# Performance work log

Measured on AMD Instinct MI355X. Metric: run time of the kernel, lower is better.

## Reference

```python
import jax, jax.numpy as jnp
import numpy as np

P = 1024          # nodes per graph
B = 64            # graphs in batch
N = P * B         # total nodes
E = N * 32        # total edges (avg degree 32)
D_IN = 16         # per-node feature dim (share_obs_dim)
H = 32            # GCN / MLP hidden dim (hardcoded in GNet)
SHARE = 64        # flat share_state dim


def setup_inputs() -> dict:
    key = jax.random.key(0)
    ks = jax.random.split(key, 20)

    x = jax.random.normal(ks[0], (N, D_IN), jnp.float32)
    src = jax.random.randint(ks[1], (E,), 0, N, dtype=jnp.int32)
    # keep edges inside each 1024-node graph block (PyG batched graphs)
    dst = (src // P) * P + jax.random.randint(ks[2], (E,), 0, P, dtype=jnp.int32)
    edge_index = jnp.stack([src, dst])
    value_batch = (jnp.arange(N, dtype=jnp.int32) // P)
    share_state = jax.random.normal(ks[3], (B, SHARE), jnp.float32)

    def lin(k, o, i):
        return jax.random.normal(k, (o, i), jnp.float32) / np.float32(np.sqrt(i))

    return {
        "x": x, "edge_index": edge_index, "value_batch": value_batch,
        "share_state": share_state,
        # value_gnet: GCNConv(D_IN,32), GCNConv(32,32), Linear(32,32), post-pool Linear(32,32)
        "W1": lin(ks[4], H, D_IN), "b1": jnp.zeros((H,), jnp.float32),
        "W2": lin(ks[5], H, H),    "b2": jnp.zeros((H,), jnp.float32),
        "Wl": lin(ks[6], H, H),    "bl": jnp.zeros((H,), jnp.float32),
        "Wp": lin(ks[7], H, H),    "bp": jnp.zeros((H,), jnp.float32),
        # value_net MLP: SHARE->32->32->32
        "Vw1": lin(ks[8], H, SHARE), "Vb1": jnp.zeros((H,), jnp.float32),
        "Vw2": lin(ks[9], H, H),     "Vb2": jnp.zeros((H,), jnp.float32),
        "Vw3": lin(ks[10], H, H),    "Vb3": jnp.zeros((H,), jnp.float32),
        # value_comnet: 64->32->1
        "Cw1": lin(ks[11], H, 2 * H), "Cb1": jnp.zeros((H,), jnp.float32),
        "Cw2": lin(ks[12], 1, H) * np.float32(0.01), "Cb2": jnp.zeros((1,), jnp.float32),
    }


def gcn_conv(x, src, dst, W, b):
    """PyG GCNConv: D^-1/2 (A+I) D^-1/2 X W^T + b (unit edge weights)."""
    n = x.shape[0]
    loop = jnp.arange(n, dtype=src.dtype)
    s = jnp.concatenate([src, loop])
    d = jnp.concatenate([dst, loop])
    deg = jax.ops.segment_sum(jnp.ones(s.shape[0], x.dtype), d, num_segments=n)
    dis = jnp.where(deg > 0, jax.lax.rsqrt(jnp.maximum(deg, 1e-12)), 0.0)
    norm = dis[s] * dis[d]                      # [E+N]
    h = x @ W.T                                  # [N, H] small GEMM first
    out = jax.ops.segment_sum(h[s] * norm[:, None], d, num_segments=n)
    return out + b


def reference(x, edge_index, value_batch, share_state,
              W1, b1, W2, b2, Wl, bl, Wp, bp,
              Vw1, Vb1, Vw2, Vb2, Vw3, Vb3,
              Cw1, Cb1, Cw2, Cb2):
    src, dst = edge_index[0], edge_index[1]
    nb = share_state.shape[0]

    # value_gnet
    h = jnp.tanh(gcn_conv(x, src, dst, W1, b1))
    h = jnp.tanh(gcn_conv(h, src, dst, W2, b2))
    h = jnp.tanh(h @ Wl.T + bl)
    pooled = jax.ops.segment_sum(h, value_batch, num_segments=nb)  # global_add_pool -> [B, 32]
    h1 = pooled @ Wp.T + bp

    # value_net MLP on flat share_state
    h2 = jnp.tanh(share_state @ Vw1.T + Vb1)
    h2 = jnp.tanh(h2 @ Vw2.T + Vb2)
    h2 = h2 @ Vw3.T + Vb3

    # value_comnet
    z = jnp.tanh(jnp.concatenate([h1, h2], axis=-1) @ Cw1.T + Cb1)
    value = z @ Cw2.T + Cb2                      # [B, 1]
    return value
```

## Files before the change

kernel.cpp:

```cpp
#include <hip/hip_runtime.h>
#include <math.h>

#define NNODES 65536
#define NEDGES 2097152
#define PGRAPH 1024
#define NGRAPH 64
#define CAPE   34560

#define OFF_GFILL 0u
#define OFF_POOL  256u
#define OFF_ROW   8704u
#define OFF_DEG   270848u
#define OFF_DIS   532992u
#define OFF_CSR   795136u
#define OFF_EBUF  5218816u
#define OFF_HBUF  14066176u

__global__ void k_bucket(const int* __restrict__ src, const int* __restrict__ dst,
                         int* __restrict__ gfill, unsigned int* __restrict__ ebuf) {
    __shared__ unsigned int sorted[8192];
    __shared__ int hist[64], lexcl[64], gbase[64], lfill[64];
    int t = threadIdx.x;
    if (t < 64) { hist[t] = 0; lfill[t] = 0; }
    __syncthreads();

    int base = blockIdx.x * 8192;
    unsigned int pk[32];
    int gg[32];
    #pragma unroll
    for (int k = 0; k < 32; k++) {
        int e = base + k * 256 + t;
        int s = src[e], d = dst[e];
        int g = s >> 10;
        pk[k] = (unsigned int)((s & 1023) | ((d & 1023) << 10) | (g << 20));
        gg[k] = g;
        atomicAdd(&hist[g], 1);
    }
    __syncthreads();
    if (t < 64) {
        int h = hist[t];
        int x = h;
        #pragma unroll
        for (int off = 1; off < 64; off <<= 1) {
            int y = __shfl_up(x, off, 64);
            if (t >= off) x += y;
        }
        lexcl[t] = x - h;
        gbase[t] = atomicAdd(&gfill[t], h);
    }
    __syncthreads();
    #pragma unroll
    for (int k = 0; k < 32; k++) {
        int g = gg[k];
        int pos = lexcl[g] + atomicAdd(&lfill[g], 1);
        sorted[pos] = pk[k];
    }
    __syncthreads();
    for (int i = t; i < 8192; i += 256) {
        unsigned int p = sorted[i];
        int g = p >> 20;
        int idx = gbase[g] + (i - lexcl[g]);
        ebuf[(size_t)g * CAPE + idx] = p;
    }
}

__global__ void k_csr(const unsigned int* __restrict__ ebuf, const int* __restrict__ gfill,
                      int* __restrict__ deg, float* __restrict__ dis,
                      int* __restrict__ row_start, unsigned short* __restrict__ csr) {
    __shared__ int ldeg[1024], lrow[1024], lfill[1024];
    __shared__ unsigned short lcsr[CAPE];
    __shared__ int wsum[16];
    int g = blockIdx.x;
    int t = threadIdx.x;
    int cnt = gfill[g];
    const unsigned int* eb = ebuf + (size_t)g * CAPE;

    ldeg[t] = 0;
    __syncthreads();
    for (int i = t; i < cnt; i += 1024) {
        unsigned int v = eb[i];
        atomicAdd(&ldeg[(v >> 10) & 1023], 1);
    }
    __syncthreads();

    int dv = ldeg[t];
    int lane = t & 63, wid = t >> 6;
    int x = dv;
    #pragma unroll
    for (int off = 1; off < 64; off <<= 1) {
        int y = __shfl_up(x, off, 64);
        if (lane >= off) x += y;
    }
    if (lane == 63) wsum[wid] = x;
    __syncthreads();
    if (t < 16) {
        int s = wsum[t];
        #pragma unroll
        for (int off = 1; off < 16; off <<= 1) {
            int y = __shfl_up(s, off, 16);
            if (t >= off) s += y;
        }
        wsum[t] = s;
    }
    __syncthreads();
    int excl = x + ((wid == 0) ? 0 : wsum[wid - 1]) - dv;

    int n = g * PGRAPH + t;
    deg[n] = dv;
    dis[n] = rsqrtf((float)(dv + 1));
    row_start[n] = g * CAPE + excl;
    lrow[t] = excl;
    lfill[t] = 0;
    __syncthreads();

    for (int i = t; i < cnt; i += 1024) {
        unsigned int v = eb[i];
        int s = v & 1023;
        int d = (v >> 10) & 1023;
        int pos = lrow[d] + atomicAdd(&lfill[d], 1);
        lcsr[pos] = (unsigned short)s;
    }
    __syncthreads();
    for (int i = t; i < cnt; i += 1024) csr[(size_t)g * CAPE + i] = lcsr[i];
}

template <int DIN, bool FINAL>
__global__ __launch_bounds__(1024, 1) void k_conv(
        const float* __restrict__ in, const float* __restrict__ W,
        const float* __restrict__ bias, const float* __restrict__ dis,
        const int* __restrict__ row_start, const int* __restrict__ deg,
        const unsigned short* __restrict__ csr,
        const float* __restrict__ Wl, const float* __restrict__ bl,
        float* __restrict__ out) {
    __shared__ float hsL[PGRAPH * 32];
    __shared__ float WlL[32 * 33];
    float4* hsL4 = (float4*)hsL;

    int t = threadIdx.x;
    int g = blockIdx.x >> 2;
    int part = blockIdx.x & 3;

    if (FINAL) { WlL[(t >> 5) * 33 + (t & 31)] = Wl[t]; }

    {
        int n = (g << 10) + t;
        float inr[DIN];
        const float4* in4 = (const float4*)(in + (size_t)n * DIN);
        #pragma unroll
        for (int k = 0; k < DIN / 4; k++) {
            float4 v = in4[k];
            inr[4*k] = v.x; inr[4*k+1] = v.y; inr[4*k+2] = v.z; inr[4*k+3] = v.w;
        }
        float dn = dis[n];
        int sw = t & 7;
        #pragma unroll
        for (int o4 = 0; o4 < 8; o4++) {
            float r[4];
            #pragma unroll
            for (int j = 0; j < 4; j++) {
                int o = o4 * 4 + j;
                float s = 0.f;
                #pragma unroll
                for (int k = 0; k < DIN; k++) s += inr[k] * W[o * DIN + k];
                r[j] = s * dn;
            }
            hsL4[t * 8 + (o4 ^ sw)] = make_float4(r[0], r[1], r[2], r[3]);
        }
    }
    __syncthreads();

    int q = t & 7;
    int grp = t >> 3;
    float4 racc[2];
    #pragma unroll
    for (int pass = 0; pass < 2; pass++) {
        int ln = part * 256 + pass * 128 + grp;
        int nn = (g << 10) + ln;
        float dnd = dis[nn];
        int st = row_start[nn];
        int d  = deg[nn];
        float4 acc = hsL4[ln * 8 + (q ^ (ln & 7))];
        for (int i = 0; i < d; i++) {
            int s = csr[st + i];
            float4 v = hsL4[s * 8 + (q ^ (s & 7))];
            acc.x += v.x; acc.y += v.y; acc.z += v.z; acc.w += v.w;
        }
        float4 bb = ((const float4*)bias)[q];
        float4 r;
        r.x = tanhf(dnd * acc.x + bb.x);
        r.y = tanhf(dnd * acc.y + bb.y);
        r.z = tanhf(dnd * acc.z + bb.z);
        r.w = tanhf(dnd * acc.w + bb.w);
        if (!FINAL) ((float4*)out)[(size_t)nn * 8 + q] = r;
        else        racc[pass] = r;
    }

    if (FINAL) {
        __syncthreads();
        #pragma unroll
        for (int pass = 0; pass < 2; pass++) {
            int lnn = pass * 128 + grp;
            hsL4[lnn * 8 + (q ^ (lnn & 7))] = racc[pass];
        }
        __syncthreads();
        int o = t & 31, seg = t >> 5;
        float ps = 0.f;
        #pragma unroll
        for (int j = 0; j < 8; j++) {
            int nl = seg * 8 + j;
            int swn = nl & 7;
            float s = bl[o];
            #pragma unroll
            for (int k = 0; k < 32; k++) {
                float h2v = hsL[nl * 32 + ((((k >> 2) ^ swn) << 2) | (k & 3))];
                s += h2v * WlL[o * 33 + k];
            }
            ps += tanhf(s);
        }
        float* psum = hsL + 8192;
        psum[t] = ps;
        __syncthreads();
        if (t < 32) {
            float tot = 0.f;
            for (int s = 0; s < 32; s++) tot += psum[s * 32 + t];
            atomicAdd(&out[g * 32 + t], tot);
        }
    }
}

__global__ void k_final(const float* __restrict__ pooled, const float* __restrict__ share,
                        const float* __restrict__ Wp,  const float* __restrict__ bp,
                        const float* __restrict__ Vw1, const float* __restrict__ Vb1,
                        const float* __restrict__ Vw2, const float* __restrict__ Vb2,
                        const float* __restrict__ Vw3, const float* __restrict__ Vb3,
                        const float* __restrict__ Cw1, const float* __restrict__ Cb1,
                        const float* __restrict__ Cw2, const float* __restrict__ Cb2,
                        float* __restrict__ out) {
    int id = blockIdx.x * 256 + threadIdx.x;
    int b = id >> 5;
    int j = id & 31;
    float p = pooled[b * 32 + j];
    float h1v = bp[j];
    #pragma unroll
    for (int k = 0; k < 32; k++) h1v += Wp[j * 32 + k] * __shfl(p, k, 32);
    float s0 = share[b * 64 + j];
    float s1 = share[b * 64 + 32 + j];
    float t1 = Vb1[j];
    #pragma unroll
    for (int k = 0; k < 32; k++) {
        t1 += Vw1[j * 64 + k] * __shfl(s0, k, 32);
        t1 += Vw1[j * 64 + 32 + k] * __shfl(s1, k, 32);
    }
    t1 = tanhf(t1);
    float t2 = Vb2[j];
    #pragma unroll
    for (int k = 0; k < 32; k++) t2 += Vw2[j * 32 + k] * __shfl(t1, k, 32);
    t2 = tanhf(t2);
    float h2v = Vb3[j];
    #pragma unroll
    for (int k = 0; k < 32; k++) h2v += Vw3[j * 32 + k] * __shfl(t2, k, 32);
    float z = Cb1[j];
    #pragma unroll
    for (int k = 0; k < 32; k++) {
        z += Cw1[j * 64 + k] * __shfl(h1v, k, 32);
        z += Cw1[j * 64 + 32 + k] * __shfl(h2v, k, 32);
    }
    z = tanhf(z);
    float v = Cw2[j] * z;
    v += __shfl_down(v, 16, 32); v += __shfl_down(v, 8, 32);
    v += __shfl_down(v, 4, 32);  v += __shfl_down(v, 2, 32);
    v += __shfl_down(v, 1, 32);
    if (j == 0) out[b] = v + Cb2[0];
}

extern "C" void kernel_launch(void* const* d_in, const int* in_sizes, int n_in,
                              void* d_out, int out_size, void* d_ws, size_t ws_size,
                              hipStream_t stream) {
    const float* x     = (const float*)d_in[0];
    const int*   ei    = (const int*)d_in[1];
    const float* share = (const float*)d_in[3];
    const float* W1 = (const float*)d_in[4];  const float* b1 = (const float*)d_in[5];
    const float* W2 = (const float*)d_in[6];  const float* b2 = (const float*)d_in[7];
    const float* Wl = (const float*)d_in[8];  const float* bl = (const float*)d_in[9];
    const float* Wp = (const float*)d_in[10]; const float* bp = (const float*)d_in[11];
    const float* Vw1 = (const float*)d_in[12]; const float* Vb1 = (const float*)d_in[13];
    const float* Vw2 = (const float*)d_in[14]; const float* Vb2 = (const float*)d_in[15];
    const float* Vw3 = (const float*)d_in[16]; const float* Vb3 = (const float*)d_in[17];
    const float* Cw1 = (const float*)d_in[18]; const float* Cb1 = (const float*)d_in[19];
    const float* Cw2 = (const float*)d_in[20]; const float* Cb2 = (const float*)d_in[21];

    char* ws = (char*)d_ws;
    int*            gfill     = (int*)(ws + OFF_GFILL);
    float*          pooled    = (float*)(ws + OFF_POOL);
    int*            row_start = (int*)(ws + OFF_ROW);
    int*            deg       = (int*)(ws + OFF_DEG);
    float*          dis       = (float*)(ws + OFF_DIS);
    unsigned short* csr       = (unsigned short*)(ws + OFF_CSR);
    unsigned int*   ebuf      = (unsigned int*)(ws + OFF_EBUF);
    float*          h1        = (float*)(ws + OFF_HBUF);

    const int* srcp = ei;
    const int* dstp = ei + NEDGES;

    hipMemsetAsync(ws, 0, 8448, stream);

    k_bucket<<<256, 256, 0, stream>>>(srcp, dstp, gfill, ebuf);
    k_csr<<<NGRAPH, 1024, 0, stream>>>(ebuf, gfill, deg, dis, row_start, csr);

    k_conv<16, false><<<256, 1024, 0, stream>>>(x,  W1, b1, dis, row_start, deg, csr,
                                                Wl, bl, h1);
    k_conv<32, true ><<<256, 1024, 0, stream>>>(h1, W2, b2, dis, row_start, deg, csr,
                                                Wl, bl, pooled);
    k_final<<<8, 256, 0, stream>>>(pooled, share, Wp, bp, Vw1, Vb1, Vw2, Vb2,
                                   Vw3, Vb3, Cw1, Cb1, Cw2, Cb2, (float*)d_out);
}
```

Measured before the change: 200.2 us.

## Fuse CSR build into first GCN conv, pad rows, fast tanh, drop pool atomics

Removes the separate CSR-building kernel. Each of the four blocks per graph now builds its own quarter of the CSR in shared memory and runs the first convolution directly from it. Rows are padded to multiples of four with a dummy zero node, so neighbour indices load as ushort4 and gather four rows per iteration. Degree and row start are packed into a single word. tanhf is replaced by an exp/rcp approximation. Pool atomics are replaced by per-block partial sums that k_final adds up. The cost is redundant edge-histogram work: every block scans the whole graph's edge list. It also loses some tanh accuracy.

```diff
diff --git a/kernel.cpp b/kernel.cpp
--- a/kernel.cpp
+++ b/kernel.cpp
@@ -5,16 +5,22 @@
 #define NEDGES 2097152
 #define PGRAPH 1024
 #define NGRAPH 64
-#define CAPE   34560
+#define CAPE_E 34560
+#define CAPQ   9728
+#define CSRG   (4 * CAPQ)
 
 #define OFF_GFILL 0u
-#define OFF_POOL  256u
-#define OFF_ROW   8704u
-#define OFF_DEG   270848u
-#define OFF_DIS   532992u
-#define OFF_CSR   795136u
-#define OFF_EBUF  5218816u
-#define OFF_HBUF  14066176u
+#define OFF_POOL4 256u
+#define OFF_ROWI  33024u
+#define OFF_DIS   295168u
+#define OFF_CSR   557312u
+#define OFF_EBUF  5538048u
+#define OFF_H1    14385408u
+
+__device__ __forceinline__ float ftanh(float x) {
+    float e = __expf(2.f * x);
+    return 1.f - 2.f * __builtin_amdgcn_rcpf(e + 1.f);
+}
 
 __global__ void k_bucket(const int* __restrict__ src, const int* __restrict__ dst,
                          int* __restrict__ gfill, unsigned int* __restrict__ ebuf) {
@@ -24,17 +30,21 @@
     if (t < 64) { hist[t] = 0; lfill[t] = 0; }
     __syncthreads();
 
-    int base = blockIdx.x * 8192;
+    const int4* src4 = (const int4*)(src + blockIdx.x * 8192);
+    const int4* dst4 = (const int4*)(dst + blockIdx.x * 8192);
     unsigned int pk[32];
-    int gg[32];
-    #pragma unroll
-    for (int k = 0; k < 32; k++) {
-        int e = base + k * 256 + t;
-        int s = src[e], d = dst[e];
-        int g = s >> 10;
-        pk[k] = (unsigned int)((s & 1023) | ((d & 1023) << 10) | (g << 20));
-        gg[k] = g;
-        atomicAdd(&hist[g], 1);
+    #pragma unroll
+    for (int k = 0; k < 8; k++) {
+        int4 s4 = src4[k * 256 + t];
+        int4 d4 = dst4[k * 256 + t];
+        int ss[4] = { s4.x, s4.y, s4.z, s4.w };
+        int dd[4] = { d4.x, d4.y, d4.z, d4.w };
+        #pragma unroll
+        for (int j = 0; j < 4; j++) {
+            int g = ss[j] >> 10;
+            pk[k * 4 + j] = (unsigned int)((ss[j] & 1023) | ((dd[j] & 1023) << 10) | (g << 20));
+            atomicAdd(&hist[g], 1);
+        }
     }
     __syncthreads();
     if (t < 64) {
@@ -51,7 +61,7 @@
     __syncthreads();
     #pragma unroll
     for (int k = 0; k < 32; k++) {
-        int g = gg[k];
+        int g = pk[k] >> 20;
         int pos = lexcl[g] + atomicAdd(&lfill[g], 1);
         sorted[pos] = pk[k];
     }
@@ -59,99 +69,91 @@
     for (int i = t; i < 8192; i += 256) {
         unsigned int p = sorted[i];
         int g = p >> 20;
-        int idx = gbase[g] + (i - lexcl[g]);
-        ebuf[(size_t)g * CAPE + idx] = p;
-    }
-}
-
-__global__ void k_csr(const unsigned int* __restrict__ ebuf, const int* __restrict__ gfill,
-                      int* __restrict__ deg, float* __restrict__ dis,
-                      int* __restrict__ row_start, unsigned short* __restrict__ csr) {
-    __shared__ int ldeg[1024], lrow[1024], lfill[1024];
-    __shared__ unsigned short lcsr[CAPE];
-    __shared__ int wsum[16];
-    int g = blockIdx.x;
+        ebuf[(size_t)g * CAPE_E + gbase[g] + (i - lexcl[g])] = p;
+    }
+}
+
+__global__ __launch_bounds__(1024, 1) void k_build_conv1(
+        const float* __restrict__ x, const float* __restrict__ W,
+        const float* __restrict__ bias,
+        const unsigned int* __restrict__ ebuf, const int* __restrict__ gfill,
+        float* __restrict__ disg, unsigned int* __restrict__ rowinfo,
+        unsigned short* __restrict__ csr, float* __restrict__ h1) {
+    __shared__ float hsL[1025 * 32];
+    __shared__ unsigned short lcsr[CAPQ];
+    __shared__ int uhist[1024];
+    __shared__ int lrow[256], lfill[256];
+    __shared__ int wsum[4];
+    float4* hsL4 = (float4*)hsL;
+
     int t = threadIdx.x;
+    int g = blockIdx.x >> 2, part = blockIdx.x & 3;
     int cnt = gfill[g];
-    const unsigned int* eb = ebuf + (size_t)g * CAPE;
-
-    ldeg[t] = 0;
-    __syncthreads();
+    const unsigned int* eb = ebuf + (size_t)g * CAPE_E;
+
+    uhist[t] = 0;
+    if (t < 32) hsL[1024 * 32 + t] = 0.f;
+    __syncthreads();
+    for (int i = t; i < cnt; i += 1024) atomicAdd(&uhist[(eb[i] >> 10) & 1023], 1);
+    __syncthreads();
+
+    int dv_own = uhist[t];
+    float dis_own = rsqrtf((float)(dv_own + 1));
+
+    int dq = 0, r4 = 0;
+    if (t < 256) { dq = uhist[part * 256 + t]; r4 = (dq + 3) & ~3; }
+    int lane = t & 63, wid = t >> 6;
+    int xx = r4;
+    #pragma unroll
+    for (int off = 1; off < 64; off <<= 1) {
+        int y = __shfl_up(xx, off, 64);
+        if (lane >= off) xx += y;
+    }
+    if (t < 256 && lane == 63) wsum[wid] = xx;
+    __syncthreads();
+    if (t < 256) {
+        int pre = 0;
+        for (int w = 0; w < wid; w++) pre += wsum[w];
+        lrow[t] = pre + xx - r4;
+        lfill[t] = 0;
+    }
+    __syncthreads();
+
     for (int i = t; i < cnt; i += 1024) {
         unsigned int v = eb[i];
-        atomicAdd(&ldeg[(v >> 10) & 1023], 1);
-    }
-    __syncthreads();
-
-    int dv = ldeg[t];
-    int lane = t & 63, wid = t >> 6;
-    int x = dv;
-    #pragma unroll
-    for (int off = 1; off < 64; off <<= 1) {
-        int y = __shfl_up(x, off, 64);
-        if (lane >= off) x += y;
-    }
-    if (lane == 63) wsum[wid] = x;
-    __syncthreads();
-    if (t < 16) {
-        int s = wsum[t];
-        #pragma unroll
-        for (int off = 1; off < 16; off <<= 1) {
-            int y = __shfl_up(s, off, 16);
-            if (t >= off) s += y;
-        }
-        wsum[t] = s;
-    }
-    __syncthreads();
-    int excl = x + ((wid == 0) ? 0 : wsum[wid - 1]) - dv;
-
-    int n = g * PGRAPH + t;
-    deg[n] = dv;
-    dis[n] = rsqrtf((float)(dv + 1));
-    row_start[n] = g * CAPE + excl;
-    lrow[t] = excl;
-    lfill[t] = 0;
-    __syncthreads();
-
-    for (int i = t; i < cnt; i += 1024) {
-        unsigned int v = eb[i];
-        int s = v & 1023;
         int d = (v >> 10) & 1023;
-        int pos = lrow[d] + atomicAdd(&lfill[d], 1);
-        lcsr[pos] = (unsigned short)s;
-    }
-    __syncthreads();
-    for (int i = t; i < cnt; i += 1024) csr[(size_t)g * CAPE + i] = lcsr[i];
-}
-
-template <int DIN, bool FINAL>
-__global__ __launch_bounds__(1024, 1) void k_conv(
-        const float* __restrict__ in, const float* __restrict__ W,
-        const float* __restrict__ bias, const float* __restrict__ dis,
-        const int* __restrict__ row_start, const int* __restrict__ deg,
-        const unsigned short* __restrict__ csr,
-        const float* __restrict__ Wl, const float* __restrict__ bl,
-        float* __restrict__ out) {
-    __shared__ float hsL[PGRAPH * 32];
-    __shared__ float WlL[32 * 33];
-    float4* hsL4 = (float4*)hsL;
-
-    int t = threadIdx.x;
-    int g = blockIdx.x >> 2;
-    int part = blockIdx.x & 3;
-
-    if (FINAL) { WlL[(t >> 5) * 33 + (t & 31)] = Wl[t]; }
+        if ((d >> 8) == part) {
+            int dl = d & 255;
+            int pos = lrow[dl] + atomicAdd(&lfill[dl], 1);
+            lcsr[pos] = (unsigned short)(v & 1023);
+        }
+    }
+    __syncthreads();
+    if (t < 256) {
+        int st = lrow[t];
+        for (int i = dq; i < r4; i++) lcsr[st + i] = 1024;
+        int n = (g << 10) + part * 256 + t;
+        disg[n] = rsqrtf((float)(dq + 1));
+        rowinfo[n] = ((unsigned int)st << 16) | (unsigned int)dq;
+    }
+    __syncthreads();
+
+    int qlen = lrow[255] + ((uhist[part * 256 + 255] + 3) & ~3);
+    {
+        const ushort4* l4 = (const ushort4*)lcsr;
+        ushort4* c4 = (ushort4*)(csr + (size_t)g * CSRG + part * CAPQ);
+        for (int i = t; i < (qlen >> 2); i += 1024) c4[i] = l4[i];
+    }
 
     {
         int n = (g << 10) + t;
-        float inr[DIN];
-        const float4* in4 = (const float4*)(in + (size_t)n * DIN);
-        #pragma unroll
-        for (int k = 0; k < DIN / 4; k++) {
+        float inr[16];
+        const float4* in4 = (const float4*)(x + (size_t)n * 16);
+        #pragma unroll
+        for (int k = 0; k < 4; k++) {
             float4 v = in4[k];
             inr[4*k] = v.x; inr[4*k+1] = v.y; inr[4*k+2] = v.z; inr[4*k+3] = v.w;
         }
-        float dn = dis[n];
         int sw = t & 7;
         #pragma unroll
         for (int o4 = 0; o4 < 8; o4++) {
@@ -161,7 +163,82 @@
                 int o = o4 * 4 + j;
                 float s = 0.f;
                 #pragma unroll
-                for (int k = 0; k < DIN; k++) s += inr[k] * W[o * DIN + k];
+                for (int k = 0; k < 16; k++) s += inr[k] * W[o * 16 + k];
+                r[j] = s * dis_own;
+            }
+            hsL4[t * 8 + (o4 ^ sw)] = make_float4(r[0], r[1], r[2], r[3]);
+        }
+    }
+    __syncthreads();
+
+    int q = t & 7, grp = t >> 3;
+    #pragma unroll
+    for (int pass = 0; pass < 2; pass++) {
+        int lq = pass * 128 + grp;
+        int ln = part * 256 + lq;
+        int d = uhist[ln];
+        float dn = rsqrtf((float)(d + 1));
+        int st = lrow[lq];
+        float4 acc = hsL4[ln * 8 + (q ^ (ln & 7))];
+        const ushort4* c4 = (const ushort4*)(lcsr + st);
+        int d4 = (d + 3) >> 2;
+        for (int i = 0; i < d4; i++) {
+            ushort4 ss = c4[i];
+            float4 v0 = hsL4[ss.x * 8 + (q ^ (ss.x & 7))];
+            float4 v1 = hsL4[ss.y * 8 + (q ^ (ss.y & 7))];
+            float4 v2 = hsL4[ss.z * 8 + (q ^ (ss.z & 7))];
+            float4 v3 = hsL4[ss.w * 8 + (q ^ (ss.w & 7))];
+            acc.x += (v0.x + v1.x) + (v2.x + v3.x);
+            acc.y += (v0.y + v1.y) + (v2.y + v3.y);
+            acc.z += (v0.z + v1.z) + (v2.z + v3.z);
+            acc.w += (v0.w + v1.w) + (v2.w + v3.w);
+        }
+        float4 bb = ((const float4*)bias)[q];
+        float4 r;
+        r.x = ftanh(dn * acc.x + bb.x);
+        r.y = ftanh(dn * acc.y + bb.y);
+        r.z = ftanh(dn * acc.z + bb.z);
+        r.w = ftanh(dn * acc.w + bb.w);
+        ((float4*)h1)[((size_t)(g << 10) + ln) * 8 + q] = r;
+    }
+}
+
+__global__ __launch_bounds__(1024, 1) void k_conv2(
+        const float* __restrict__ h1, const float* __restrict__ W,
+        const float* __restrict__ bias, const float* __restrict__ disg,
+        const unsigned int* __restrict__ rowinfo, const unsigned short* __restrict__ csr,
+        const float* __restrict__ Wl, const float* __restrict__ bl,
+        float* __restrict__ pooled4) {
+    __shared__ float hsL[1025 * 32];
+    __shared__ float WlL[32 * 33];
+    float4* hsL4 = (float4*)hsL;
+
+    int t = threadIdx.x;
+    int g = blockIdx.x >> 2, part = blockIdx.x & 3;
+
+    if (t < 32 * 32) WlL[(t >> 5) * 33 + (t & 31)] = Wl[t];
+    if (t < 32) hsL[1024 * 32 + t] = 0.f;
+
+    {
+        int n = (g << 10) + t;
+        float inr[32];
+        const float4* in4 = (const float4*)(h1 + (size_t)n * 32);
+        #pragma unroll
+        for (int k = 0; k < 8; k++) {
+            float4 v = in4[k];
+            inr[4*k] = v.x; inr[4*k+1] = v.y; inr[4*k+2] = v.z; inr[4*k+3] = v.w;
+        }
+        float dn = disg[n];
+        int sw = t & 7;
+        #pragma unroll
+        for (int o4 = 0; o4 < 8; o4++) {
+            float r[4];
+            #pragma unroll
+            for (int j = 0; j < 4; j++) {
+                int o = o4 * 4 + j;
+                float s = 0.f;
+                #pragma unroll
+                for (int k = 0; k < 32; k++) s += inr[k] * W[o * 32 + k];
                 r[j] = s * dn;
             }
             hsL4[t * 8 + (o4 ^ sw)] = make_float4(r[0], r[1], r[2], r[3]);
@@ -169,66 +246,72 @@
     }
     __syncthreads();
 
-    int q = t & 7;
-    int grp = t >> 3;
+    int q = t & 7, grp = t >> 3;
     float4 racc[2];
     #pragma unroll
     for (int pass = 0; pass < 2; pass++) {
-        int ln = part * 256 + pass * 128 + grp;
-        int nn = (g << 10) + ln;
-        float dnd = dis[nn];
-        int st = row_start[nn];
-        int d  = deg[nn];
+        int lq = pass * 128 + grp;
+        int ln = part * 256 + lq;
+        int n = (g << 10) + ln;
+        unsigned int ri = rowinfo[n];
+        int st = ri >> 16;
+        int d  = ri & 0xFFFF;
+        float dn = rsqrtf((float)(d + 1));
         float4 acc = hsL4[ln * 8 + (q ^ (ln & 7))];
-        for (int i = 0; i < d; i++) {
-            int s = csr[st + i];
-            float4 v = hsL4[s * 8 + (q ^ (s & 7))];
-            acc.x += v.x; acc.y += v.y; acc.z += v.z; acc.w += v.w;
+        const ushort4* c4 = (const ushort4*)(csr + (size_t)g * CSRG + part * CAPQ + st);
+        int d4 = (d + 3) >> 2;
+        for (int i = 0; i < d4; i++) {
+            ushort4 ss = c4[i];
+            float4 v0 = hsL4[ss.x * 8 + (q ^ (ss.x & 7))];
+            float4 v1 = hsL4[ss.y * 8 + (q ^ (ss.y & 7))];
+            float4 v2 = hsL4[ss.z * 8 + (q ^ (ss.z & 7))];
+            float4 v3 = hsL4[ss.w * 8 + (q ^ (ss.w & 7))];
+            acc.x += (v0.x + v1.x) + (v2.x + v3.x);
+            acc.y += (v0.y + v1.y) + (v2.y + v3.y);
+            acc.z += (v0.z + v1.z) + (v2.z + v3.z);
+            acc.w += (v0.w + v1.w) + (v2.w + v3.w);
         }
         float4 bb = ((const float4*)bias)[q];
         float4 r;
-        r.x = tanhf(dnd * acc.x + bb.x);
-        r.y = tanhf(dnd * acc.y + bb.y);
-        r.z = tanhf(dnd * acc.z + bb.z);
-        r.w = tanhf(dnd * acc.w + bb.w);
-        if (!FINAL) ((float4*)out)[(size_t)nn * 8 + q] = r;
-        else        racc[pass] = r;
-    }
-
-    if (FINAL) {
-        __syncthreads();
-        #pragma unroll
-        for (int pass = 0; pass < 2; pass++) {
-            int lnn = pass * 128 + grp;
-            hsL4[lnn * 8 + (q ^ (lnn & 7))] = racc[pass];
-        }
-        __syncthreads();
-        int o = t & 31, seg = t >> 5;
-        float ps = 0.f;
-        #pragma unroll
-        for (int j = 0; j < 8; j++) {
-            int nl = seg * 8 + j;
-            int swn = nl & 7;
-            float s = bl[o];
-            #pragma unroll
-            for (int k = 0; k < 32; k++) {
-                float h2v = hsL[nl * 32 + ((((k >> 2) ^ swn) << 2) | (k & 3))];
-                s += h2v * WlL[o * 33 + k];
-            }
-            ps += tanhf(s);
-        }
-        float* psum = hsL + 8192;
-        psum[t] = ps;
-        __syncthreads();
-        if (t < 32) {
-            float tot = 0.f;
-            for (int s = 0; s < 32; s++) tot += psum[s * 32 + t];
-            atomicAdd(&out[g * 32 + t], tot);
-        }
-    }
-}
-
-__global__ void k_final(const float* __restrict__ pooled, const float* __restrict__ share,
+        r.x = ftanh(dn * acc.x + bb.x);
+        r.y = ftanh(dn * acc.y + bb.y);
+        r.z = ftanh(dn * acc.z + bb.z);
+        r.w = ftanh(dn * acc.w + bb.w);
+        racc[pass] = r;
+    }
+
+    __syncthreads();
+    #pragma unroll
+    for (int pass = 0; pass < 2; pass++) {
+        int lnn = pass * 128 + grp;
+        hsL4[lnn * 8 + (q ^ (lnn & 7))] = racc[pass];
+    }
+    __syncthreads();
+    int o = t & 31, seg = t >> 5;
+    float ps = 0.f;
+    #pragma unroll
+    for (int j = 0; j < 8; j++) {
+        int nl = seg * 8 + j;
+        int swn = nl & 7;
+        float s = bl[o];
+        #pragma unroll
+        for (int k = 0; k < 32; k++) {
+            float h2v = hsL[nl * 32 + ((((k >> 2) ^ swn) << 2) | (k & 3))];
+            s += h2v * WlL[o * 33 + k];
+        }
+        ps += ftanh(s);
+    }
+    float* psum = hsL + 8192;
+    psum[t] = ps;
+    __syncthreads();
+    if (t < 32) {
+        float tot = 0.f;
+        for (int s = 0; s < 32; s++) tot += psum[s * 32 + t];
+        pooled4[blockIdx.x * 32 + t] = tot;
+    }
+}
+
+__global__ void k_final(const float* __restrict__ pooled4, const float* __restrict__ share,
                         const float* __restrict__ Wp,  const float* __restrict__ bp,
                         const float* __restrict__ Vw1, const float* __restrict__ Vb1,
                         const float* __restrict__ Vw2, const float* __restrict__ Vb2,
@@ -239,7 +322,8 @@
     int id = blockIdx.x * 256 + threadIdx.x;
     int b = id >> 5;
     int j = id & 31;
-    float p = pooled[b * 32 + j];
+    float p = pooled4[(b * 4 + 0) * 32 + j] + pooled4[(b * 4 + 1) * 32 + j]
+            + pooled4[(b * 4 + 2) * 32 + j] + pooled4[(b * 4 + 3) * 32 + j];
     float h1v = bp[j];
     #pragma unroll
     for (int k = 0; k < 32; k++) h1v += Wp[j * 32 + k] * __shfl(p, k, 32);
@@ -290,27 +374,24 @@
     const float* Cw2 = (const float*)d_in[20]; const float* Cb2 = (const float*)d_in[21];
 
     char* ws = (char*)d_ws;
-    int*            gfill     = (int*)(ws + OFF_GFILL);
-    float*          pooled    = (float*)(ws + OFF_POOL);
-    int*            row_start = (int*)(ws + OFF_ROW);
-    int*            deg       = (int*)(ws + OFF_DEG);
-    float*          dis       = (float*)(ws + OFF_DIS);
-    unsigned short* csr       = (unsigned short*)(ws + OFF_CSR);
-    unsigned int*   ebuf      = (unsigned int*)(ws + OFF_EBUF);
-    float*          h1        = (float*)(ws + OFF_HBUF);
+    int*            gfill   = (int*)(ws + OFF_GFILL);
+    float*          pooled4 = (float*)(ws + OFF_POOL4);
+    unsigned int*   rowinfo = (unsigned int*)(ws + OFF_ROWI);
+    float*          disg    = (float*)(ws + OFF_DIS);
+    unsigned short* csr     = (unsigned short*)(ws + OFF_CSR);
+    unsigned int*   ebuf    = (unsigned int*)(ws + OFF_EBUF);
+    float*          h1      = (float*)(ws + OFF_H1);
 
     const int* srcp = ei;
     const int* dstp = ei + NEDGES;
 
-    hipMemsetAsync(ws, 0, 8448, stream);
+    hipMemsetAsync(gfill, 0, 256, stream);
 
     k_bucket<<<256, 256, 0, stream>>>(srcp, dstp, gfill, ebuf);
-    k_csr<<<NGRAPH, 1024, 0, stream>>>(ebuf, gfill, deg, dis, row_start, csr);
-
-    k_conv<16, false><<<256, 1024, 0, stream>>>(x,  W1, b1, dis, row_start, deg, csr,
-                                                Wl, bl, h1);
-    k_conv<32, true ><<<256, 1024, 0, stream>>>(h1, W2, b2, dis, row_start, deg, csr,
-                                                Wl, bl, pooled);
-    k_final<<<8, 256, 0, stream>>>(pooled, share, Wp, bp, Vw1, Vb1, Vw2, Vb2,
+    k_build_conv1<<<256, 1024, 0, stream>>>(x, W1, b1, ebuf, gfill,
+                                            disg, rowinfo, csr, h1);
+    k_conv2<<<256, 1024, 0, stream>>>(h1, W2, b2, disg, rowinfo, csr,
+                                      Wl, bl, pooled4);
+    k_final<<<8, 256, 0, stream>>>(pooled4, share, Wp, bp, Vw1, Vb1, Vw2, Vb2,
                                    Vw3, Vb3, Cw1, Cb1, Cw2, Cb2, (float*)d_out);
 }
```

New measurement: 191.5 us. 1.05x faster.
